# Performance work log

Measured on AMD Instinct MI355X. Metric: run time of the kernel, lower is better.

Reference implementation:

```python
import jax, jax.numpy as jnp
import numpy as np

D_MODEL = 2048
NUM_HEADS = 16
NUM_KV_HEADS = 4
D_HEAD = D_MODEL // NUM_HEADS  # 128
GROUPS = NUM_HEADS // NUM_KV_HEADS  # 4
ROPE_THETA = 10000.0
EPS = 1e-6


def setup_inputs() -> dict:
    key = jax.random.key(0)
    ks = jax.random.split(key, 7)
    B, S = 2, 2048
    s = 1.0 / np.sqrt(D_MODEL)
    return {
        "qkv": jax.random.normal(ks[0], (B, S, D_MODEL), dtype=jnp.float32),
        "Wq": jax.random.normal(ks[1], (D_MODEL, D_MODEL), dtype=jnp.float32) * s,
        "Wk": jax.random.normal(ks[2], (NUM_KV_HEADS * D_HEAD, D_MODEL), dtype=jnp.float32) * s,
        "Wv": jax.random.normal(ks[3], (NUM_KV_HEADS * D_HEAD, D_MODEL), dtype=jnp.float32) * s,
        "Wo": jax.random.normal(ks[4], (D_MODEL, D_MODEL), dtype=jnp.float32) * s,
        "q_gamma": jnp.ones((D_HEAD,), dtype=jnp.float32),
        "k_gamma": jnp.ones((D_HEAD,), dtype=jnp.float32),
    }


def _rmsnorm(x, gamma):
    # per-head RMSNorm over last dim (d_head)
    var = jnp.mean(jnp.square(x), axis=-1, keepdims=True)
    return x * jax.lax.rsqrt(var + EPS) * gamma


def _rope(x, cos, sin):
    # x: [B, S, H, Dh]; cos/sin: [S, Dh]
    half = x.shape[-1] // 2
    x1, x2 = x[..., :half], x[..., half:]
    rot = jnp.concatenate([-x2, x1], axis=-1)
    return x * cos[None, :, None, :] + rot * sin[None, :, None, :]


def reference(qkv, Wq, Wk, Wv, Wo, q_gamma, k_gamma):
    B, S, D = qkv.shape
    q = jnp.einsum("bsd,ed->bse", qkv, Wq).reshape(B, S, NUM_HEADS, D_HEAD)
    k = jnp.einsum("bsd,ed->bse", qkv, Wk).reshape(B, S, NUM_KV_HEADS, D_HEAD)
    v = jnp.einsum("bsd,ed->bse", qkv, Wv).reshape(B, S, NUM_KV_HEADS, D_HEAD)

    q = _rmsnorm(q, q_gamma)
    k = _rmsnorm(k, k_gamma)

    # RoPE, position_ids = arange(S)
    pos = jnp.arange(S, dtype=jnp.float32)
    inv_freq = 1.0 / (ROPE_THETA ** (jnp.arange(0, D_HEAD, 2, dtype=jnp.float32) / D_HEAD))
    ang = pos[:, None] * inv_freq[None, :]                 # [S, Dh/2]
    cos = jnp.concatenate([jnp.cos(ang), jnp.cos(ang)], axis=-1)  # [S, Dh]
    sin = jnp.concatenate([jnp.sin(ang), jnp.sin(ang)], axis=-1)
    q = _rope(q, cos, sin)
    k = _rope(k, cos, sin)

    # [B, H, S, Dh]
    q = q.transpose(0, 2, 1, 3)
    k = k.transpose(0, 2, 1, 3)
    v = v.transpose(0, 2, 1, 3)
    # GQA: repeat kv heads
    k = jnp.repeat(k, GROUPS, axis=1)
    v = jnp.repeat(v, GROUPS, axis=1)

    scale = 1.0 / np.sqrt(D_HEAD)
    scores = jnp.einsum("bhqd,bhkd->bhqk", q, k) * scale
    causal = jnp.tril(jnp.ones((S, S), dtype=bool))
    scores = jnp.where(causal[None, None], scores, jnp.finfo(scores.dtype).min)
    probs = jax.nn.softmax(scores, axis=-1)
    attended = jnp.einsum("bhqk,bhkd->bhqd", probs, v)     # [B, H, S, Dh]
    attended = attended.transpose(0, 2, 1, 3).reshape(B, S, D)
    return jnp.einsum("bsd,ed->bse", attended, Wo)
```

## Files before the change

### kernel.cpp

```cpp
#include <hip/hip_runtime.h>

#define S_LEN 2048
#define B_SZ 2
#define DMODEL 2048
#define NHEADS 16
#define NKV 4
#define DHEAD 128
#define SCALE 0.08838834764831845f
#define KVB 32

typedef __bf16 bf16x8 __attribute__((ext_vector_type(8)));
typedef __bf16 bf16x4 __attribute__((ext_vector_type(4)));
typedef float f32x4 __attribute__((ext_vector_type(4)));

#define MFMA(a, b, c) __builtin_amdgcn_mfma_f32_16x16x32_bf16(a, b, c, 0, 0, 0)

__device__ __forceinline__ void gload_lds16(const __bf16* g, __bf16* l) {
    __builtin_amdgcn_global_load_lds(
        (const __attribute__((address_space(1))) unsigned int*)g,
        (__attribute__((address_space(3))) unsigned int*)l, 16, 0, 0);
}

__global__ void rope_tables_kernel(float* __restrict__ cosT, float* __restrict__ sinT) {
    int i = blockIdx.x * 256 + threadIdx.x;
    int s = i >> 6, d = i & 63;
    float freq = powf(10000.0f, -(2.0f * (float)d) / 128.0f);
    float ang = (float)s * freq;
    cosT[i] = cosf(ang);
    sinT[i] = sinf(ang);
}

__global__ __launch_bounds__(256) void convert_kernel(
    const float* __restrict__ s0, const float* __restrict__ s1,
    const float* __restrict__ s2, const float* __restrict__ s3,
    const float* __restrict__ s4,
    __bf16* __restrict__ d0, __bf16* __restrict__ d1, __bf16* __restrict__ d2,
    __bf16* __restrict__ d3, __bf16* __restrict__ d4) {
    const float* s;
    __bf16* d;
    int n8;
    switch (blockIdx.y) {
        case 0: s = s0; d = d0; n8 = (B_SZ * S_LEN * DMODEL) / 8; break;
        case 1: s = s1; d = d1; n8 = (DMODEL * DMODEL) / 8; break;
        case 2: s = s2; d = d2; n8 = (NKV * DHEAD * DMODEL) / 8; break;
        case 3: s = s3; d = d3; n8 = (NKV * DHEAD * DMODEL) / 8; break;
        default: s = s4; d = d4; n8 = (DMODEL * DMODEL) / 8; break;
    }
    for (int i = blockIdx.x * 256 + threadIdx.x; i < n8; i += 512 * 256) {
        float4 a = ((const float4*)s)[2 * i];
        float4 b = ((const float4*)s)[2 * i + 1];
        bf16x8 o = {(__bf16)a.x, (__bf16)a.y, (__bf16)a.z, (__bf16)a.w,
                    (__bf16)b.x, (__bf16)b.y, (__bf16)b.z, (__bf16)b.w};
        *(bf16x8*)&d[i * 8] = o;
    }
}

template <int BM>
__device__ __forceinline__ void gemm256(const __bf16* __restrict__ A,
                                        const __bf16* __restrict__ W,
                                        int bm, int bn, int K,
                                        f32x4 (&acc)[BM / 32][4],
                                        __bf16* arena) {
    constexpr int MI = BM / 32;
    constexpr int ALT = BM / 64;
    __bf16* As = arena;
    __bf16* Bs = arena + 2 * BM * 64;
    const int tid = threadIdx.x;
    const int lane = tid & 63;
    const int wave = tid >> 6;
    const int lr = lane & 15, lk = lane >> 4;
    const int wr = wave >> 2;
    const int wc = wave & 3;
    const int sRow = lane >> 3;
    const int sCol = 8 * ((lane & 7) ^ sRow);

    auto stageA = [&](int bi, int k0) {
#pragma unroll
        for (int it = 0; it < ALT; ++it) {
            const int row = it * 64 + wave * 8 + sRow;
            gload_lds16(A + (size_t)(bm + row) * K + k0 + sCol,
                        As + bi * BM * 64 + it * 4096 + wave * 512);
        }
    };
    auto stageB = [&](int bi, int k0) {
#pragma unroll
        for (int it = 0; it < 4; ++it) {
            const int row = it * 64 + wave * 8 + sRow;
            gload_lds16(W + (size_t)(bn + row) * K + k0 + sCol,
                        Bs + bi * 16384 + it * 4096 + wave * 512);
        }
    };

#pragma unroll
    for (int mi = 0; mi < MI; ++mi)
#pragma unroll
        for (int ni = 0; ni < 4; ++ni) acc[mi][ni] = (f32x4){0.f, 0.f, 0.f, 0.f};

    const int NT = K >> 6;
    stageA(0, 0);
    stageB(0, 0);
    stageA(1, 64);
    stageB(1, 64);
    if constexpr (BM == 256) asm volatile("s_waitcnt vmcnt(8)" ::: "memory");
    else                     asm volatile("s_waitcnt vmcnt(6)" ::: "memory");
    __builtin_amdgcn_s_barrier();

    for (int t = 0; t < NT; ++t) {
        const int bi = t & 1;
#pragma unroll
        for (int kk = 0; kk < 2; ++kk) {
            bf16x8 af[MI], bfr[4];
#pragma unroll
            for (int i = 0; i < MI; ++i) {
                const int r = wr * (BM / 2) + i * 16 + lr;
                const int slot = (kk * 4 + lk) ^ (r & 7);
                af[i] = *(const bf16x8*)&As[bi * BM * 64 + r * 64 + slot * 8];
            }
#pragma unroll
            for (int i = 0; i < 4; ++i) {
                const int r = wc * 64 + i * 16 + lr;
                const int slot = (kk * 4 + lk) ^ (r & 7);
                bfr[i] = *(const bf16x8*)&Bs[bi * 16384 + r * 64 + slot * 8];
            }
#pragma unroll
            for (int mi = 0; mi < MI; ++mi)
#pragma unroll
                for (int ni = 0; ni < 4; ++ni)
                    acc[mi][ni] = MFMA(af[mi], bfr[ni], acc[mi][ni]);
        }
        asm volatile("s_waitcnt lgkmcnt(0)" ::: "memory");
        __builtin_amdgcn_sched_barrier(0);
        __builtin_amdgcn_s_barrier();
        if (t + 2 < NT) {
            stageA(bi, (t + 2) * 64);
            stageB(bi, (t + 2) * 64);
        }
        if (t + 1 < NT) {
            if (t + 2 < NT) {
                if constexpr (BM == 256) asm volatile("s_waitcnt vmcnt(8)" ::: "memory");
                else                     asm volatile("s_waitcnt vmcnt(6)" ::: "memory");
            } else {
                asm volatile("s_waitcnt vmcnt(0)" ::: "memory");
            }
            __builtin_amdgcn_s_barrier();
        }
    }
}

__global__ __launch_bounds__(512, 2) void qkv_proj_kernel(
    const __bf16* __restrict__ qkvb, const __bf16* __restrict__ Wq,
    const __bf16* __restrict__ Wk, const __bf16* __restrict__ Wv,
    const float* __restrict__ qg, const float* __restrict__ kg,
    const float* __restrict__ cosT, const float* __restrict__ sinT,
    __bf16* __restrict__ qb, __bf16* __restrict__ kb, __bf16* __restrict__ vt) {
    __shared__ alignas(16) __bf16 arena[4 * 256 * 64];
    const int id = (blockIdx.x & 7) * 24 + (blockIdx.x >> 3);
    const int bmi = id / 12, bni = id % 12;
    const int bm = bmi * 256;
    const __bf16* W;
    int bn;
    if (bni < 8)       { W = Wq; bn = bni * 256; }
    else if (bni < 10) { W = Wk; bn = (bni - 8) * 256; }
    else               { W = Wv; bn = (bni - 10) * 256; }

    f32x4 acc[8][4];
    gemm256<256>(qkvb, W, bm, bn, 2048, acc, arena);

    const int tid = threadIdx.x;
    const int lane = tid & 63, wave = tid >> 6;
    const int lr = lane & 15, lk = lane >> 4;
    const int wr = wave >> 2, wc = wave & 3;
    const int dc0 = (wc & 1) * 64;

    if (bni < 10) {
        const bool isQ = (bni < 8);
        const float* gamma = isQ ? qg : kg;
        const float scl = isQ ? SCALE : 1.0f;
        const int hh = (isQ ? bni * 2 : (bni - 8) * 2) + (wc >> 1);
        const int nh = isQ ? NHEADS : NKV;
        __bf16* outb = isQ ? qb : kb;
        float g[4];
#pragma unroll
        for (int ni = 0; ni < 4; ++ni) g[ni] = gamma[dc0 + ni * 16 + lr];

        float* xbuf = (float*)arena;
        float* ssbuf = (float*)((char*)arena + 70 * 1024);

        float rs[8][4];
#pragma unroll
        for (int mi = 0; mi < 8; ++mi)
#pragma unroll
            for (int r = 0; r < 4; ++r) {
                float ss = 0.f;
#pragma unroll
                for (int ni = 0; ni < 4; ++ni) ss += acc[mi][ni][r] * acc[mi][ni][r];
                ss += __shfl_xor(ss, 1);
                ss += __shfl_xor(ss, 2);
                ss += __shfl_xor(ss, 4);
                ss += __shfl_xor(ss, 8);
                if (lr == 0) ssbuf[wc * 256 + wr * 128 + mi * 16 + lk * 4 + r] = ss;
            }
        __syncthreads();
#pragma unroll
        for (int mi = 0; mi < 8; ++mi)
#pragma unroll
            for (int r = 0; r < 4; ++r) {
                const int rowl = wr * 128 + mi * 16 + lk * 4 + r;
                const float tot = ssbuf[wc * 256 + rowl] + ssbuf[(wc ^ 1) * 256 + rowl];
                rs[mi][r] = rsqrtf(tot * (1.0f / 128.0f) + 1e-6f) * scl;
            }
        __syncthreads();

#pragma unroll
        for (int ch = 0; ch < 4; ++ch) {
            float y[2][4][4];
#pragma unroll
            for (int m2 = 0; m2 < 2; ++m2)
#pragma unroll
                for (int ni = 0; ni < 4; ++ni)
#pragma unroll
                    for (int r = 0; r < 4; ++r) {
                        const int mi = ch * 2 + m2;
                        y[m2][ni][r] = acc[mi][ni][r] * rs[mi][r] * g[ni];
                        xbuf[tid * 33 + m2 * 16 + ni * 4 + r] = y[m2][ni][r];
                    }
            __syncthreads();
            float yp[2][4][4];
#pragma unroll
            for (int m2 = 0; m2 < 2; ++m2)
#pragma unroll
                for (int ni = 0; ni < 4; ++ni)
#pragma unroll
                    for (int r = 0; r < 4; ++r)
                        yp[m2][ni][r] = xbuf[(tid ^ 64) * 33 + m2 * 16 + ni * 4 + r];
#pragma unroll
            for (int m2 = 0; m2 < 2; ++m2)
#pragma unroll
                for (int r = 0; r < 4; ++r) {
                    const int mi = ch * 2 + m2;
                    const int gm = bm + wr * 128 + mi * 16 + lk * 4 + r;
                    const int bb = gm >> 11, s = gm & 2047;
                    const float* ct = cosT + s * 64;
                    const float* st = sinT + s * 64;
                    __bf16* orow = outb + (((size_t)(bb * nh + hh)) * S_LEN + s) * DHEAD;
#pragma unroll
                    for (int ni = 0; ni < 4; ++ni) {
                        const int dd = ni * 16 + lr;
                        const float c = ct[dd], sn = st[dd];
                        const float own = y[m2][ni][r], par = yp[m2][ni][r];
                        const float o = (wc & 1) ? (own * c + par * sn)
                                                 : (own * c - par * sn);
                        orow[dc0 + dd] = (__bf16)o;
                    }
                }
            __syncthreads();
        }
    } else {
        const int kvh = (bni - 10) * 2 + (wc >> 1);
#pragma unroll
        for (int mi = 0; mi < 8; ++mi) {
            const int gm = bm + wr * 128 + mi * 16 + lk * 4;
            const int bb = gm >> 11, s0 = gm & 2047;
            __bf16* vbase = vt + ((size_t)(bb * NKV + kvh)) * DHEAD * S_LEN;
#pragma unroll
            for (int ni = 0; ni < 4; ++ni) {
                const int d = dc0 + ni * 16 + lr;
                bf16x4 pk = {(__bf16)acc[mi][ni][0], (__bf16)acc[mi][ni][1],
                             (__bf16)acc[mi][ni][2], (__bf16)acc[mi][ni][3]};
                *(bf16x4*)&vbase[(size_t)d * S_LEN + s0] = pk;
            }
        }
    }
}

__global__ __launch_bounds__(512, 2) void out_proj_kernel(
    const __bf16* __restrict__ att, const __bf16* __restrict__ Wo,
    float* __restrict__ out) {
    __shared__ alignas(16) __bf16 arena[2 * 128 * 64 + 2 * 256 * 64];
    const int id = (blockIdx.x & 7) * 32 + (blockIdx.x >> 3);
    const int bm = (id >> 3) * 128, bn = (id & 7) * 256;

    f32x4 acc[4][4];
    gemm256<128>(att, Wo, bm, bn, 2048, acc, arena);

    const int lane = threadIdx.x & 63, wave = threadIdx.x >> 6;
    const int lr = lane & 15, lk = lane >> 4;
    const int wr = wave >> 2, wc = wave & 3;
#pragma unroll
    for (int mi = 0; mi < 4; ++mi)
#pragma unroll
        for (int ni = 0; ni < 4; ++ni)
#pragma unroll
            for (int r = 0; r < 4; ++r) {
                const int row = bm + wr * 64 + mi * 16 + lk * 4 + r;
                const int col = bn + wc * 64 + ni * 16 + lr;
                out[(size_t)row * DMODEL + col] = acc[mi][ni][r];
            }
}

__global__ __launch_bounds__(256, 2) void flash_kernel(
    const __bf16* __restrict__ qb, const __bf16* __restrict__ kb,
    const __bf16* __restrict__ vt, __bf16* __restrict__ att) {
    __shared__ alignas(16) __bf16 K_lds[2][32 * 128];
    __shared__ alignas(16) __bf16 V_lds[2][128 * 32];
    __shared__ alignas(16) __bf16 p_lds[4][16][40];

    const int bh = blockIdx.x;
    const int b = bh >> 4, h = bh & 15, kv = h >> 2;
    const int j = blockIdx.y;
    const int lane = threadIdx.x & 63, wave = threadIdx.x >> 6;
    const int lr = lane & 15, lk = lane >> 4;

    const int qloB = j * 64 + wave * 16;
    const int qhiB = (31 - j) * 64 + wave * 16;
    const int ntL  = ((qloB + 15) >> 5) + 1;
    const int ntHw = ((qhiB + 15) >> 5) + 1;
    const int ntH  = 64 - 2 * j;

    const __bf16* Qp = qb + ((size_t)(b * NHEADS + h)) * S_LEN * DHEAD;
    const __bf16* Kp = kb + ((size_t)(b * NKV + kv)) * S_LEN * DHEAD;
    const __bf16* Vt = vt + ((size_t)(b * NKV + kv)) * DHEAD * S_LEN;

    bf16x8 qlo[4], qhi[4];
#pragma unroll
    for (int f = 0; f < 4; ++f) {
        qlo[f] = *(const bf16x8*)&Qp[(size_t)(qloB + lr) * DHEAD + f * 32 + lk * 8];
        qhi[f] = *(const bf16x8*)&Qp[(size_t)(qhiB + lr) * DHEAD + f * 32 + lk * 8];
    }

    const int c0 = 2 * wave;
    const int l4 = lane >> 4, l15 = lane & 15;
    const int l2 = lane >> 2, l3 = lane & 3;
    const int vcol = ((l3 ^ (l2 & 3)) << 3);

    auto stage = [&](int bufi, int t) {
        const int k0s = t * KVB;
#pragma unroll
        for (int i = 0; i < 2; ++i) {
            const int c = c0 + i;
            const int rK = c * 4 + l4;
            const int kcol = ((l15 ^ (rK & 7)) << 3);
            gload_lds16(Kp + (size_t)(k0s + rK) * DHEAD + kcol, &K_lds[bufi][c * 512]);
            const int rV = c * 16 + l2;
            gload_lds16(Vt + (size_t)rV * S_LEN + k0s + vcol, &V_lds[bufi][c * 512]);
        }
    };

    f32x4 accL[8] = {}, accH[8] = {};
    float lsumL[4] = {0.f, 0.f, 0.f, 0.f}, lsumH[4] = {0.f, 0.f, 0.f, 0.f};
    const int swzK = (lr & 7) << 4;
    const int swzV = (lr & 3) << 4;

    auto frag_step = [&](const bf16x8 (&qf)[4], int qbase, f32x4 (&acc)[8],
                         float (&lsum)[4], const bf16x8 (&kf)[8],
                         const bf16x8 (&vf)[8], int k0) {
        f32x4 sc[2] = {};
        __builtin_amdgcn_s_setprio(1);
#pragma unroll
        for (int kk = 0; kk < 2; ++kk)
#pragma unroll
            for (int f = 0; f < 4; ++f)
                sc[kk] = MFMA(qf[f], kf[kk * 4 + f], sc[kk]);
        __builtin_amdgcn_s_setprio(0);
        asm volatile("s_waitcnt lgkmcnt(0)" ::: "memory");
#pragma unroll
        for (int r = 0; r < 4; ++r) {
            const int qr = qbase + lk * 4 + r;
            float s0 = sc[0][r], s1 = sc[1][r];
            if (k0 + lr > qr) s0 = -1e30f;
            if (k0 + 16 + lr > qr) s1 = -1e30f;
            float p0 = __expf(s0), p1 = __expf(s1);
            lsum[r] += p0 + p1;
            p_lds[wave][lk * 4 + r][lr] = (__bf16)p0;
            p_lds[wave][lk * 4 + r][lr + 16] = (__bf16)p1;
        }
        asm volatile("s_waitcnt lgkmcnt(0)" ::: "memory");
        bf16x8 pf = *(const bf16x8*)&p_lds[wave][lr][lk * 8];
        __builtin_amdgcn_s_setprio(1);
#pragma unroll
        for (int nf = 0; nf < 8; ++nf)
            acc[nf] = MFMA(pf, vf[nf], acc[nf]);
        __builtin_amdgcn_s_setprio(0);
    };

    int cur = 0;
    stage(0, 0);
    __syncthreads();
    for (int t = 0; t < ntH; ++t) {
        if (t + 1 < ntH) stage(cur ^ 1, t + 1);
        const int k0 = t * KVB;
        bf16x8 kf[8], vf[8];
#pragma unroll
        for (int kk = 0; kk < 2; ++kk)
#pragma unroll
            for (int f = 0; f < 4; ++f) {
                const int cb = (f * 64 + lk * 16) ^ swzK;
                kf[kk * 4 + f] =
                    *(const bf16x8*)((const char*)&K_lds[cur][(kk * 16 + lr) * 128] + cb);
            }
#pragma unroll
        for (int nf = 0; nf < 8; ++nf) {
            const int cb = (lk * 16) ^ swzV;
            vf[nf] = *(const bf16x8*)((const char*)&V_lds[cur][(nf * 16 + lr) * 32] + cb);
        }
        if (t < ntHw) frag_step(qhi, qhiB, accH, lsumH, kf, vf, k0);
        if (t < ntL)  frag_step(qlo, qloB, accL, lsumL, kf, vf, k0);
        __syncthreads();
        cur ^= 1;
    }

#pragma unroll
    for (int r = 0; r < 4; ++r) {
#pragma unroll
        for (int m = 1; m < 16; m <<= 1) {
            lsumL[r] += __shfl_xor(lsumL[r], m);
            lsumH[r] += __shfl_xor(lsumH[r], m);
        }
    }
#pragma unroll
    for (int nf = 0; nf < 8; ++nf)
#pragma unroll
        for (int r = 0; r < 4; ++r) {
            int qrL = qloB + lk * 4 + r;
            int qrH = qhiB + lk * 4 + r;
            att[((size_t)(b * S_LEN) + qrL) * DMODEL + h * DHEAD + nf * 16 + lr] =
                (__bf16)(accL[nf][r] / lsumL[r]);
            att[((size_t)(b * S_LEN) + qrH) * DMODEL + h * DHEAD + nf * 16 + lr] =
                (__bf16)(accH[nf][r] / lsumH[r]);
        }
}

extern "C" void kernel_launch(void* const* d_in, const int* in_sizes, int n_in,
                              void* d_out, int out_size, void* d_ws, size_t ws_size,
                              hipStream_t stream) {
    const float* qkv = (const float*)d_in[0];
    const float* Wq  = (const float*)d_in[1];
    const float* Wk  = (const float*)d_in[2];
    const float* Wv  = (const float*)d_in[3];
    const float* Wo  = (const float*)d_in[4];
    const float* qg  = (const float*)d_in[5];
    const float* kg  = (const float*)d_in[6];
    float* out = (float*)d_out;

    size_t off = 0;
    char* wsb = (char*)d_ws;
    auto alloc = [&](size_t n) {
        char* p = wsb + off;
        off += (n + 255) & ~(size_t)255;
        return (void*)p;
    };
    const size_t M = (size_t)B_SZ * S_LEN;
    float* cosT   = (float*)alloc((size_t)S_LEN * 64 * 4);
    float* sinT   = (float*)alloc((size_t)S_LEN * 64 * 4);
    __bf16* qb    = (__bf16*)alloc((size_t)B_SZ * NHEADS * S_LEN * DHEAD * 2);
    __bf16* kb    = (__bf16*)alloc((size_t)B_SZ * NKV * S_LEN * DHEAD * 2);
    __bf16* vt    = (__bf16*)alloc((size_t)B_SZ * NKV * DHEAD * S_LEN * 2);
    __bf16* att   = (__bf16*)alloc(M * DMODEL * 2);
    __bf16* qkv_b = (__bf16*)alloc(M * DMODEL * 2);
    __bf16* wq_b  = (__bf16*)alloc((size_t)DMODEL * DMODEL * 2);
    __bf16* wk_b  = (__bf16*)alloc((size_t)NKV * DHEAD * DMODEL * 2);
    __bf16* wv_b  = (__bf16*)alloc((size_t)NKV * DHEAD * DMODEL * 2);
    __bf16* wo_b  = (__bf16*)alloc((size_t)DMODEL * DMODEL * 2);

    rope_tables_kernel<<<(S_LEN * 64) / 256, 256, 0, stream>>>(cosT, sinT);
    convert_kernel<<<dim3(512, 5), 256, 0, stream>>>(qkv, Wq, Wk, Wv, Wo,
                                                     qkv_b, wq_b, wk_b, wv_b, wo_b);
    qkv_proj_kernel<<<192, 512, 0, stream>>>(qkv_b, wq_b, wk_b, wv_b,
                                             qg, kg, cosT, sinT, qb, kb, vt);
    flash_kernel<<<dim3(B_SZ * NHEADS, 16), 256, 0, stream>>>(qb, kb, vt, att);
    out_proj_kernel<<<256, 512, 0, stream>>>(att, wo_b, out);
}
```

Before: 195.3 us.

## Interleave GEMM LDS reads, MFMA quarters and global staging; fold RoPE tables into convert

The GEMM main loop now reads both k-halves of the B fragments up front and splits the A-fragment reads and MFMA work into four quarters. The global-to-LDS staging for the next tiles is placed between the later quarters, and MFMA sections run under raised wave priority, so loads overlap with matrix math instead of waiting at one barrier. The RoPE table generation moves into an extra blockIdx.y slice of the convert kernel, which removes one kernel launch. In exchange the loop has more barriers per iteration and keeps more fragments live in registers, which could hurt occupancy.

```diff
diff --git a/kernel.cpp b/kernel.cpp
--- a/kernel.cpp
+++ b/kernel.cpp
@@ -21,21 +21,22 @@
         (__attribute__((address_space(3))) unsigned int*)l, 16, 0, 0);
 }
 
-__global__ void rope_tables_kernel(float* __restrict__ cosT, float* __restrict__ sinT) {
-    int i = blockIdx.x * 256 + threadIdx.x;
-    int s = i >> 6, d = i & 63;
-    float freq = powf(10000.0f, -(2.0f * (float)d) / 128.0f);
-    float ang = (float)s * freq;
-    cosT[i] = cosf(ang);
-    sinT[i] = sinf(ang);
-}
-
 __global__ __launch_bounds__(256) void convert_kernel(
     const float* __restrict__ s0, const float* __restrict__ s1,
     const float* __restrict__ s2, const float* __restrict__ s3,
     const float* __restrict__ s4,
     __bf16* __restrict__ d0, __bf16* __restrict__ d1, __bf16* __restrict__ d2,
-    __bf16* __restrict__ d3, __bf16* __restrict__ d4) {
+    __bf16* __restrict__ d3, __bf16* __restrict__ d4,
+    float* __restrict__ cosT, float* __restrict__ sinT) {
+    if (blockIdx.y == 5) {
+        int i = blockIdx.x * 256 + threadIdx.x;
+        int s = i >> 6, d = i & 63;
+        float freq = powf(10000.0f, -(2.0f * (float)d) / 128.0f);
+        float ang = (float)s * freq;
+        cosT[i] = cosf(ang);
+        sinT[i] = sinf(ang);
+        return;
+    }
     const float* s;
     __bf16* d;
     int n8;
@@ -63,6 +64,7 @@
                                         __bf16* arena) {
     constexpr int MI = BM / 32;
     constexpr int ALT = BM / 64;
+    constexpr int QM = MI / 4;
     __bf16* As = arena;
     __bf16* Bs = arena + 2 * BM * 64;
     const int tid = threadIdx.x;
@@ -107,34 +109,58 @@
 
     for (int t = 0; t < NT; ++t) {
         const int bi = t & 1;
-#pragma unroll
-        for (int kk = 0; kk < 2; ++kk) {
-            bf16x8 af[MI], bfr[4];
-#pragma unroll
-            for (int i = 0; i < MI; ++i) {
-                const int r = wr * (BM / 2) + i * 16 + lr;
-                const int slot = (kk * 4 + lk) ^ (r & 7);
-                af[i] = *(const bf16x8*)&As[bi * BM * 64 + r * 64 + slot * 8];
-            }
-#pragma unroll
-            for (int i = 0; i < 4; ++i) {
+        bf16x8 af[MI][2], bfr[4][2];
+        auto rdA = [&](int i, int kk) {
+            const int r = wr * (BM / 2) + i * 16 + lr;
+            const int slot = (kk * 4 + lk) ^ (r & 7);
+            af[i][kk] = *(const bf16x8*)&As[bi * BM * 64 + r * 64 + slot * 8];
+        };
+        auto quad = [&](int q) {
+            __builtin_amdgcn_s_setprio(1);
+#pragma unroll
+            for (int mi = q * QM; mi < (q + 1) * QM; ++mi)
+#pragma unroll
+                for (int kk = 0; kk < 2; ++kk)
+#pragma unroll
+                    for (int ni = 0; ni < 4; ++ni)
+                        acc[mi][ni] = MFMA(af[mi][kk], bfr[ni][kk], acc[mi][ni]);
+            __builtin_amdgcn_s_setprio(0);
+        };
+
+#pragma unroll
+        for (int i = 0; i < 4; ++i)
+#pragma unroll
+            for (int kk = 0; kk < 2; ++kk) {
                 const int r = wc * 64 + i * 16 + lr;
                 const int slot = (kk * 4 + lk) ^ (r & 7);
-                bfr[i] = *(const bf16x8*)&Bs[bi * 16384 + r * 64 + slot * 8];
-            }
-#pragma unroll
-            for (int mi = 0; mi < MI; ++mi)
-#pragma unroll
-                for (int ni = 0; ni < 4; ++ni)
-                    acc[mi][ni] = MFMA(af[mi], bfr[ni], acc[mi][ni]);
-        }
+                bfr[i][kk] = *(const bf16x8*)&Bs[bi * 16384 + r * 64 + slot * 8];
+            }
+#pragma unroll
+        for (int i = 0; i < QM; ++i)
+#pragma unroll
+            for (int kk = 0; kk < 2; ++kk) rdA(i, kk);
+        __builtin_amdgcn_s_barrier();
         asm volatile("s_waitcnt lgkmcnt(0)" ::: "memory");
         __builtin_amdgcn_sched_barrier(0);
+        quad(0);
         __builtin_amdgcn_s_barrier();
-        if (t + 2 < NT) {
-            stageA(bi, (t + 2) * 64);
-            stageB(bi, (t + 2) * 64);
-        }
+
+#pragma unroll
+        for (int i = QM; i < MI; ++i)
+#pragma unroll
+            for (int kk = 0; kk < 2; ++kk) rdA(i, kk);
+        __builtin_amdgcn_s_barrier();
+        asm volatile("s_waitcnt lgkmcnt(0)" ::: "memory");
+        __builtin_amdgcn_sched_barrier(0);
+        quad(1);
+        __builtin_amdgcn_s_barrier();
+
+        if (t + 2 < NT) stageA(bi, (t + 2) * 64);
+        quad(2);
+        __builtin_amdgcn_s_barrier();
+
+        if (t + 2 < NT) stageB(bi, (t + 2) * 64);
+        quad(3);
         if (t + 1 < NT) {
             if (t + 2 < NT) {
                 if constexpr (BM == 256) asm volatile("s_waitcnt vmcnt(8)" ::: "memory");
@@ -462,9 +488,9 @@
     __bf16* wv_b  = (__bf16*)alloc((size_t)NKV * DHEAD * DMODEL * 2);
     __bf16* wo_b  = (__bf16*)alloc((size_t)DMODEL * DMODEL * 2);
 
-    rope_tables_kernel<<<(S_LEN * 64) / 256, 256, 0, stream>>>(cosT, sinT);
-    convert_kernel<<<dim3(512, 5), 256, 0, stream>>>(qkv, Wq, Wk, Wv, Wo,
-                                                     qkv_b, wq_b, wk_b, wv_b, wo_b);
+    convert_kernel<<<dim3(512, 6), 256, 0, stream>>>(qkv, Wq, Wk, Wv, Wo,
+                                                     qkv_b, wq_b, wk_b, wv_b, wo_b,
+                                                     cosT, sinT);
     qkv_proj_kernel<<<192, 512, 0, stream>>>(qkv_b, wq_b, wk_b, wv_b,
                                              qg, kg, cosT, sinT, qb, kb, vt);
     flash_kernel<<<dim3(B_SZ * NHEADS, 16), 256, 0, stream>>>(qb, kb, vt, att);
```

Result: faster. 185.7 us (median of 3 runs) (-4.9%).
